# Performance work log

Measured on AMD Instinct MI355X. Metric: run time of the kernel, lower is better.

Reference implementation:

```python
import jax, jax.numpy as jnp
import numpy as np

GROUP = 64  # hardcoded group_size in the module


def setup_inputs() -> dict:
    key = jax.random.key(0)
    ks = jax.random.split(key, 7)
    B, S, K, N, R = 64, 1, 4096, 12288, 32
    G = K // GROUP
    x = jax.random.normal(ks[0], (B, S, K), jnp.float32)
    # int4 weight residual values in [-8, 7]
    q_w = jax.random.randint(ks[1], (N, K), -8, 8, jnp.int32)
    # per-(group, out_channel) positive scales, shape [G, N] as in the module buffer
    wscales = jax.random.uniform(ks[2], (G, N), jnp.float32, 1e-3, 2e-2)
    lora_down = jax.random.normal(ks[3], (K, R), jnp.float32) * 0.02
    lora_up = jax.random.normal(ks[4], (N, R), jnp.float32) * 0.02
    smooth = jax.random.uniform(ks[5], (K,), jnp.float32, 0.5, 2.0)
    bias = jax.random.normal(ks[6], (N,), jnp.float32) * 0.01
    return {"x": x, "q_w": q_w, "wscales": wscales, "lora_down": lora_down,
            "lora_up": lora_up, "smooth": smooth, "bias": bias}


def reference(x, q_w, wscales, lora_down, lora_up, smooth, bias):
    # x: [B, S, K]; q_w: [N, K] int4 values; wscales: [K//64, N]
    B, S, K = x.shape
    G = K // GROUP
    # smoothing divide (per in-channel)
    x_div = x / smooth  # [B, S, K]
    # --- activation W4A4 path: symmetric int4 per-token per-group quantization ---
    xg = x_div.reshape(B, S, G, GROUP)
    ascale = jnp.maximum(jnp.max(jnp.abs(xg), axis=-1) / 7.0, 1e-8)  # [B, S, G]
    xq = jnp.clip(jnp.round(xg / ascale[..., None]), -8.0, 7.0)
    x_deq = (xq * ascale[..., None]).reshape(B, S, K)  # dequantized activation
    # --- dequantize int4 weight residual: w[n,k] = q[n,k] * wscales[k//64, n] ---
    w_deq = q_w.astype(jnp.float32) * jnp.repeat(wscales, GROUP, axis=0).T  # [N, K]
    # main quantized GEMM
    y = jnp.einsum('bsk,nk->bsn', x_deq, w_deq)  # [B, S, N]
    # low-rank SVD branch on the full-precision smoothed activation
    y = y + (x_div @ lora_down) @ lora_up.T
    y = y + bias
    return y
```

## Files before the change

### kernel.cpp

```cpp
#include <hip/hip_runtime.h>
#include <hip/hip_bf16.h>

#define K_DIM 4096
#define N_DIM 12288
#define B_DIM 64
#define G_DIM 64
#define R_DIM 32
#define NT_DIM 768
#define GPB 16

typedef int v4i __attribute__((ext_vector_type(4)));

__device__ __forceinline__ int pack4(const v4i a) {
    return (a.x & 255) | ((a.y & 255) << 8) | ((a.z & 255) << 16) | (a.w << 24);
}

__global__ __launch_bounds__(256) void quant_lora_kernel(
    const float* __restrict__ x, const float* __restrict__ smooth,
    const float* __restrict__ ld, char* __restrict__ xq_p,
    float* __restrict__ ascale, float* __restrict__ t_part) {
    const int b = blockIdx.x >> 4;
    const int kc = blockIdx.x & 15;
    const int tid = threadIdx.x;
    const int k = kc * 256 + tid;

    __shared__ float sx[256];
    __shared__ float red[256];

    const float xd = x[b * K_DIM + k] / smooth[k];
    sx[tid] = xd;

    const int lane = tid & 63;
    float a = fabsf(xd);
    #pragma unroll
    for (int off = 32; off; off >>= 1) a = fmaxf(a, __shfl_xor(a, off));
    const float as = fmaxf(a / 7.0f, 1e-8f);
    float q = rintf(xd / as);
    q = fminf(fmaxf(q, -8.0f), 7.0f);
    const int g = kc * 4 + (tid >> 6);
    const int bt = b >> 4, b15 = b & 15;
    const int quad = lane >> 4, kin = lane & 15;
    xq_p[((((size_t)bt * G_DIM + g) * 64) + quad * 16 + b15) * 16 + kin] = (char)(int)q;
    if (lane == 0) ascale[b * G_DIM + g] = as;
    __syncthreads();

    const int r = tid & 31, c = tid >> 5;
    const int kb = kc * 256 + c * 32;
    float acc = 0.f;
    #pragma unroll 8
    for (int kk = 0; kk < 32; ++kk)
        acc += sx[c * 32 + kk] * ld[(size_t)(kb + kk) * R_DIM + r];
    red[tid] = acc;
    __syncthreads();
    if (tid < 32) {
        float s = 0.f;
        #pragma unroll
        for (int c2 = 0; c2 < 8; ++c2) s += red[c2 * 32 + tid];
        t_part[kc * (B_DIM * R_DIM) + b * R_DIM + tid] = s;
    }
}

__global__ __launch_bounds__(256) void treduce_kernel(
    const float* __restrict__ t_part, float* __restrict__ t) {
    const int i = blockIdx.x * 256 + threadIdx.x;
    float s = 0.f;
    #pragma unroll
    for (int kc = 0; kc < 16; ++kc) s += t_part[kc * (B_DIM * R_DIM) + i];
    t[i] = s;
}

__global__ __launch_bounds__(256) void main_ksplit_kernel(
    const int* __restrict__ qw, const float* __restrict__ wscales,
    const v4i* __restrict__ xq_p, const float* __restrict__ ascale,
    float* __restrict__ psum) {
    __shared__ float s_ws[GPB * 16];
    __shared__ float s_as[GPB * 68];

    const int bid = blockIdx.x;
    const int nt = bid >> 2, kc = bid & 3;
    const int n0 = nt * 16, g0 = kc * GPB;
    const int tid = threadIdx.x;

    if (tid < GPB * 16)
        s_ws[tid] = wscales[(g0 + (tid >> 4)) * N_DIM + n0 + (tid & 15)];
    #pragma unroll
    for (int i = tid; i < B_DIM * GPB; i += 256) {
        const int b = i & 63, gl = i >> 6;
        s_as[gl * 68 + b] = ascale[b * G_DIM + g0 + gl];
    }
    __syncthreads();

    const int w = tid >> 6, lane = tid & 63;
    const int col = lane & 15, quad = lane >> 4;

    float facc[4] = {0.f, 0.f, 0.f, 0.f};
    const v4i zero = {0, 0, 0, 0};
    const v4i* xbase = xq_p + (size_t)w * G_DIM * 64 + lane;
    const int* bsrc = qw + (size_t)(n0 + col) * K_DIM + quad * 16;

    #pragma unroll 2
    for (int gl = 0; gl < GPB; ++gl) {
        const int g = g0 + gl;
        const int* p = bsrc + g * 64;
        const v4i a0 = *(const v4i*)(p);
        const v4i a1 = *(const v4i*)(p + 4);
        const v4i a2 = *(const v4i*)(p + 8);
        const v4i a3 = *(const v4i*)(p + 12);
        v4i bq;
        bq.x = pack4(a0); bq.y = pack4(a1); bq.z = pack4(a2); bq.w = pack4(a3);
        const v4i xa = xbase[(size_t)g * 64];
        const v4i d = __builtin_amdgcn_mfma_i32_16x16x64_i8(xa, bq, zero, 0, 0, 0);
        const float wsc = s_ws[gl * 16 + col];
        const float4 as4 = *(const float4*)&s_as[gl * 68 + w * 16 + quad * 4];
        facc[0] = fmaf(as4.x * wsc, (float)d[0], facc[0]);
        facc[1] = fmaf(as4.y * wsc, (float)d[1], facc[1]);
        facc[2] = fmaf(as4.z * wsc, (float)d[2], facc[2]);
        facc[3] = fmaf(as4.w * wsc, (float)d[3], facc[3]);
    }

    float* pp = psum + (size_t)kc * B_DIM * N_DIM;
    #pragma unroll
    for (int r = 0; r < 4; ++r) {
        const int b = w * 16 + quad * 4 + r;
        pp[(size_t)b * N_DIM + n0 + col] = facc[r];
    }
}

__global__ __launch_bounds__(256) void final_kernel(
    const float* __restrict__ psum, const float* __restrict__ t,
    const float* __restrict__ lora_up, const float* __restrict__ bias,
    float* __restrict__ out) {
    __shared__ float s_t[B_DIM * R_DIM];
    const int n0 = blockIdx.x * 64;
    const int tid = threadIdx.x;
    for (int i = tid; i < B_DIM * R_DIM; i += 256) s_t[i] = t[i];
    __syncthreads();

    const int n = n0 + (tid & 63);
    const int bq = tid >> 6;
    float4 lu[8];
    {
        const float4* lp = (const float4*)(lora_up + (size_t)n * R_DIM);
        #pragma unroll
        for (int i = 0; i < 8; ++i) lu[i] = lp[i];
    }
    const float bs = bias[n];
    #pragma unroll 4
    for (int r = 0; r < 16; ++r) {
        const int b = bq * 16 + r;
        float acc = bs;
        #pragma unroll
        for (int kc = 0; kc < 4; ++kc)
            acc += psum[((size_t)kc * B_DIM + b) * N_DIM + n];
        #pragma unroll
        for (int r2 = 0; r2 < 8; ++r2) {
            const float4 tv = *(const float4*)&s_t[b * R_DIM + r2 * 4];
            acc += tv.x * lu[r2].x + tv.y * lu[r2].y +
                   tv.z * lu[r2].z + tv.w * lu[r2].w;
        }
        out[(size_t)b * N_DIM + n] = acc;
    }
}

extern "C" void kernel_launch(void* const* d_in, const int* in_sizes, int n_in,
                              void* d_out, int out_size, void* d_ws, size_t ws_size,
                              hipStream_t stream) {
    const float* x         = (const float*)d_in[0];
    const int*   q_w       = (const int*)d_in[1];
    const float* wscales   = (const float*)d_in[2];
    const float* lora_down = (const float*)d_in[3];
    const float* lora_up   = (const float*)d_in[4];
    const float* smooth    = (const float*)d_in[5];
    const float* bias      = (const float*)d_in[6];
    float* out = (float*)d_out;

    char*  xq     = (char*)d_ws;
    float* ascale = (float*)((char*)d_ws + 262144);
    float* t_part = (float*)((char*)d_ws + 262144 + 16384);
    float* t      = (float*)((char*)d_ws + 409600);
    float* psum   = (float*)((char*)d_ws + 417792);

    quant_lora_kernel<<<B_DIM * 16, 256, 0, stream>>>(x, smooth, lora_down,
                                                      xq, ascale, t_part);
    treduce_kernel<<<8, 256, 0, stream>>>(t_part, t);
    main_ksplit_kernel<<<NT_DIM * 4, 256, 0, stream>>>(q_w, wscales,
                                                       (const v4i*)xq, ascale,
                                                       psum);
    final_kernel<<<N_DIM / 64, 256, 0, stream>>>(psum, t, lora_up, bias, out);
}
```

Baseline: 348.4 us.

## Assign distinct n-tiles per wave and reuse weights across all batch tiles

Each wave now handles its own 16-column output tile and loops over all four batch tiles, so each int4 weight element is loaded from global memory once instead of once per wave. Weight loads are reorganized for row-contiguous coalesced access and transposed through a swizzled per-wave LDS buffer into MFMA operand layout. The grid shrinks fourfold, trading fewer blocks and more accumulator registers for removal of redundant weight traffic.

```diff
diff --git a/kernel.cpp b/kernel.cpp
--- a/kernel.cpp
+++ b/kernel.cpp
@@ -73,16 +73,20 @@
     const int* __restrict__ qw, const float* __restrict__ wscales,
     const v4i* __restrict__ xq_p, const float* __restrict__ ascale,
     float* __restrict__ psum) {
-    __shared__ float s_ws[GPB * 16];
+    __shared__ float s_ws[4 * GPB * 16];
     __shared__ float s_as[GPB * 68];
+    __shared__ int   s_pw[4][256];
 
     const int bid = blockIdx.x;
-    const int nt = bid >> 2, kc = bid & 3;
-    const int n0 = nt * 16, g0 = kc * GPB;
+    const int ntb = bid >> 2, kc = bid & 3;
+    const int g0 = kc * GPB;
     const int tid = threadIdx.x;
 
-    if (tid < GPB * 16)
-        s_ws[tid] = wscales[(g0 + (tid >> 4)) * N_DIM + n0 + (tid & 15)];
+    #pragma unroll
+    for (int i = tid; i < 4 * GPB * 16; i += 256) {
+        const int w2 = i >> 8, gl = (i >> 4) & 15, c = i & 15;
+        s_ws[i] = wscales[(g0 + gl) * N_DIM + (ntb * 4 + w2) * 16 + c];
+    }
     #pragma unroll
     for (int i = tid; i < B_DIM * GPB; i += 256) {
         const int b = i & 63, gl = i >> 6;
@@ -91,39 +95,62 @@
     __syncthreads();
 
     const int w = tid >> 6, lane = tid & 63;
+    const int nt = ntb * 4 + w;
+    const int n0 = nt * 16;
     const int col = lane & 15, quad = lane >> 4;
 
-    float facc[4] = {0.f, 0.f, 0.f, 0.f};
+    const int lr = lane >> 2, lc = lane & 3;
+    const int lswz = (lr >> 1) & 3;
+    const int* wsrc = qw + (size_t)(n0 + lr) * K_DIM + lc * 4;
+
+    const int rswz = (col >> 1) & 3;
+    int* const mywr = &s_pw[w][lr * 16 + lc];
+    const int* const myrd = &s_pw[w][col * 16 + (quad ^ rswz) * 4];
+
+    float facc[4][4];
+    #pragma unroll
+    for (int i = 0; i < 4; ++i)
+        #pragma unroll
+        for (int j = 0; j < 4; ++j) facc[i][j] = 0.f;
+
     const v4i zero = {0, 0, 0, 0};
-    const v4i* xbase = xq_p + (size_t)w * G_DIM * 64 + lane;
-    const int* bsrc = qw + (size_t)(n0 + col) * K_DIM + quad * 16;
+    const v4i* xgbase = xq_p + (size_t)g0 * 64 + lane;
 
     #pragma unroll 2
     for (int gl = 0; gl < GPB; ++gl) {
-        const int g = g0 + gl;
-        const int* p = bsrc + g * 64;
-        const v4i a0 = *(const v4i*)(p);
-        const v4i a1 = *(const v4i*)(p + 4);
-        const v4i a2 = *(const v4i*)(p + 8);
-        const v4i a3 = *(const v4i*)(p + 12);
-        v4i bq;
-        bq.x = pack4(a0); bq.y = pack4(a1); bq.z = pack4(a2); bq.w = pack4(a3);
-        const v4i xa = xbase[(size_t)g * 64];
-        const v4i d = __builtin_amdgcn_mfma_i32_16x16x64_i8(xa, bq, zero, 0, 0, 0);
-        const float wsc = s_ws[gl * 16 + col];
-        const float4 as4 = *(const float4*)&s_as[gl * 68 + w * 16 + quad * 4];
-        facc[0] = fmaf(as4.x * wsc, (float)d[0], facc[0]);
-        facc[1] = fmaf(as4.y * wsc, (float)d[1], facc[1]);
-        facc[2] = fmaf(as4.z * wsc, (float)d[2], facc[2]);
-        facc[3] = fmaf(as4.w * wsc, (float)d[3], facc[3]);
+        const int* p = wsrc + (g0 + gl) * 64;
+        const v4i q0 = *(const v4i*)(p);
+        const v4i q1 = *(const v4i*)(p + 16);
+        const v4i q2 = *(const v4i*)(p + 32);
+        const v4i q3 = *(const v4i*)(p + 48);
+        mywr[((0 ^ lswz) * 4)] = pack4(q0);
+        mywr[((1 ^ lswz) * 4)] = pack4(q1);
+        mywr[((2 ^ lswz) * 4)] = pack4(q2);
+        mywr[((3 ^ lswz) * 4)] = pack4(q3);
+        const v4i bq = *(const v4i*)myrd;
+        const float wsc = s_ws[(w * GPB + gl) * 16 + col];
+        #pragma unroll
+        for (int bt = 0; bt < 4; ++bt) {
+            const v4i xa = xgbase[((size_t)bt * G_DIM + gl) * 64];
+            const v4i d =
+                __builtin_amdgcn_mfma_i32_16x16x64_i8(xa, bq, zero, 0, 0, 0);
+            const float4 as4 =
+                *(const float4*)&s_as[gl * 68 + bt * 16 + quad * 4];
+            facc[bt][0] = fmaf(as4.x * wsc, (float)d[0], facc[bt][0]);
+            facc[bt][1] = fmaf(as4.y * wsc, (float)d[1], facc[bt][1]);
+            facc[bt][2] = fmaf(as4.z * wsc, (float)d[2], facc[bt][2]);
+            facc[bt][3] = fmaf(as4.w * wsc, (float)d[3], facc[bt][3]);
+        }
     }
 
     float* pp = psum + (size_t)kc * B_DIM * N_DIM;
     #pragma unroll
-    for (int r = 0; r < 4; ++r) {
-        const int b = w * 16 + quad * 4 + r;
-        pp[(size_t)b * N_DIM + n0 + col] = facc[r];
-    }
+    for (int bt = 0; bt < 4; ++bt)
+        #pragma unroll
+        for (int r = 0; r < 4; ++r) {
+            const int b = bt * 16 + quad * 4 + r;
+            pp[(size_t)b * N_DIM + n0 + col] = facc[bt][r];
+        }
 }
 
 __global__ __launch_bounds__(256) void final_kernel(
@@ -183,8 +210,8 @@
     quant_lora_kernel<<<B_DIM * 16, 256, 0, stream>>>(x, smooth, lora_down,
                                                       xq, ascale, t_part);
     treduce_kernel<<<8, 256, 0, stream>>>(t_part, t);
-    main_ksplit_kernel<<<NT_DIM * 4, 256, 0, stream>>>(q_w, wscales,
-                                                       (const v4i*)xq, ascale,
-                                                       psum);
+    main_ksplit_kernel<<<NT_DIM, 256, 0, stream>>>(q_w, wscales,
+                                                   (const v4i*)xq, ascale,
+                                                   psum);
     final_kernel<<<N_DIM / 64, 256, 0, stream>>>(psum, t, lora_up, bias, out);
 }
```

Measured after the change: 316.9 us. 9.0% less time.
